# Kernel tuning notes

Hardware: AMD Instinct MI355X
Metric: run time of the kernel (lower is better)

## Reference

```python
import jax, jax.numpy as jnp
import numpy as np

B, D, O = 65536, 512, 64   # batch, input_size, output_size
E, T, K = 8, 2, 2          # num_experts, n_task, top-k
H1, H2 = 64, 32            # expert_hidden_layers (hardcoded in Expert)
LOSS_COEF = 0.01
EPS = 1e-10


def setup_inputs() -> dict:
    key = jax.random.key(0)
    ks = jax.random.split(key, 8)
    f32 = jnp.float32
    def rn(k, shape, scale):
        return jax.random.normal(k, shape, f32) * scale
    return {
        "x": jax.random.normal(ks[0], (B, D), f32),
        # gating params (one per task); init random so top-k routing is nontrivial
        "w_gates": rn(ks[1], (T, D, E), 0.02),
        "b_gates": jnp.zeros((T, E), f32),
        # per-expert MLP params, stacked over the expert axis
        "W1": rn(ks[2], (E, D, H1), 1.0 / np.sqrt(D)),
        "b1": jnp.zeros((E, H1), f32),
        "W2": rn(ks[3], (E, H1, H2), 1.0 / np.sqrt(H1)),
        "b2": jnp.zeros((E, H2), f32),
        "W3": rn(ks[4], (E, H2, O), 1.0 / np.sqrt(H2)),
        "b3": jnp.zeros((E, O), f32),
    }


def _cv_squared(v):
    # torch .var() default is unbiased (ddof=1)
    return jnp.var(v, ddof=1) / (jnp.mean(v) ** 2 + EPS)


def reference(x, w_gates, b_gates, W1, b1, W2, b2, W3, b3):
    # --- noisy_top_k_gating in eval mode (train=False): clean logits, top-k softmax ---
    logits = jnp.einsum("bd,tde->tbe", x, w_gates) + b_gates[:, None, :]  # [T,B,E]
    top_v, top_i = jax.lax.top_k(logits, K)                                # [T,B,K]
    top_g = jax.nn.softmax(top_v, axis=-1)                                 # [T,B,K]
    # scatter top-k gate values back to dense [T,B,E] (zeros elsewhere)
    gates = jnp.sum(jax.nn.one_hot(top_i, E, dtype=top_g.dtype) * top_g[..., None], axis=2)

    # --- experts: each token through each expert MLP (gates zero out non-selected,
    #     mathematically identical to dispatch/combine) ---
    h = jax.nn.relu(jnp.einsum("bd,edh->ebh", x, W1) + b1[:, None, :])     # [E,B,H1]
    h = jax.nn.relu(jnp.einsum("ebh,eho->ebo", h, W2) + b2[:, None, :])    # [E,B,H2]
    expert_out = jax.nn.relu(jnp.einsum("ebh,eho->ebo", h, W3) + b3[:, None, :])  # [E,B,O]

    # weighted combine per task
    y = jnp.einsum("tbe,ebo->tbo", gates, expert_out)                       # [T,B,O]

    # --- load balancing loss ---
    importance = gates.sum(axis=1)                          # [T,E]
    load = (gates > 0).sum(axis=1).astype(jnp.float32)      # [T,E]
    loss = LOSS_COEF * (jax.vmap(_cv_squared)(importance) + jax.vmap(_cv_squared)(load)).sum()
    return y, loss
```

## Files before the change

### kernel.cpp

```cpp
#include <hip/hip_runtime.h>


typedef short bfrag __attribute__((ext_vector_type(8)));
typedef float facc  __attribute__((ext_vector_type(4)));

#define MFMA16(a, b, c) __builtin_amdgcn_mfma_f32_16x16x32_bf16((a), (b), (c), 0, 0, 0)

__device__ __forceinline__ unsigned short bfbits(float f) {
  unsigned int u = __builtin_bit_cast(unsigned int, f);
  u += 0x7FFFu + ((u >> 16) & 1u);
  return (unsigned short)(u >> 16);
}
__device__ __forceinline__ unsigned pack2(float a, float b) {
  return (unsigned)bfbits(a) | ((unsigned)bfbits(b) << 16);
}
__device__ __forceinline__ float bf2f(unsigned short s) {
  unsigned int u = ((unsigned int)s) << 16;
  return __builtin_bit_cast(float, u);
}

#define G_OFF   65536
#define R_OFF   70656
#define A_OFF   72704
#define SM_SIZE 72832

__global__ __launch_bounds__(512, 4) void moe_fused(
    const float* __restrict__ x,
    const float* __restrict__ b_gates,
    const float* __restrict__ wgt,
    const float* __restrict__ b1,
    const float* __restrict__ b2,
    const float* __restrict__ b3,
    const bfrag* __restrict__ w1f,
    const bfrag* __restrict__ w2f,
    const bfrag* __restrict__ w3f,
    float* __restrict__ gacc_out,
    float* __restrict__ y)
{
  __shared__ alignas(16) char smem[SM_SIZE];
  const int tid = threadIdx.x;
  const int wave = tid >> 6, lane = tid & 63;
  const int q = lane & 15, g = lane >> 4;
  const int e = wave;
  const unsigned cb = (unsigned)e * 8192u;

  if (tid < 32) ((float*)(smem + A_OFF))[tid] = 0.f;

  const float* src = x + (size_t)blockIdx.x * 64 * 512 + lane * 512 + wave * 64;
  float4 fr[16];
  #pragma unroll
  for (int j = 0; j < 16; ++j) fr[j] = ((const float4*)src)[j];

  {
    int wu = __builtin_amdgcn_readfirstlane(wave);
    const float* wbase = wgt + wu * 64;
    float* pp = (float*)(smem + wave * 4096 + lane * 64);
    #pragma unroll
    for (int te = 0; te < 16; ++te) {
      const float* wrow = wbase + te * 512;
      float a0 = 0.f, a1 = 0.f, a2 = 0.f, a3 = 0.f;
      #pragma unroll
      for (int j = 0; j < 16; ++j) {
        a0 = fmaf(fr[j].x, wrow[j * 4 + 0], a0);
        a1 = fmaf(fr[j].y, wrow[j * 4 + 1], a1);
        a2 = fmaf(fr[j].z, wrow[j * 4 + 2], a2);
        a3 = fmaf(fr[j].w, wrow[j * 4 + 3], a3);
      }
      pp[(te + lane) & 15] = (a0 + a1) + (a2 + a3);
    }
  }
  __syncthreads();

  #pragma unroll
  for (int i0 = 0; i0 < 2; ++i0) {
    int i = i0 * 512 + tid;
    int tok = i >> 4, te = i & 15;
    const float* pb = (const float*)smem + tok * 16 + ((te + tok) & 15);
    float s = 0.f;
    #pragma unroll
    for (int w2 = 0; w2 < 8; ++w2) s += pb[w2 * 1024];
    ((float*)(smem + G_OFF))[tok * 20 + te] = s + b_gates[te];
  }
  __syncthreads();

  #pragma unroll
  for (int p = 0; p < 8; ++p) {
    uint4 v;
    v.x = pack2(fr[2 * p].x, fr[2 * p].y);
    v.y = pack2(fr[2 * p].z, fr[2 * p].w);
    v.z = pack2(fr[2 * p + 1].x, fr[2 * p + 1].y);
    v.w = pack2(fr[2 * p + 1].z, fr[2 * p + 1].w);
    unsigned byte = ((unsigned)(lane * 1024 + wave * 128 + p * 16)) ^ ((unsigned)(lane & 7) << 4);
    *(uint4*)(smem + byte) = v;
  }

  if (tid < 128) {
    int tok = tid >> 1, task = tid & 1;
    const float* Gr = (const float*)(smem + G_OFF) + tok * 20 + task * 8;
    float l[8];
    #pragma unroll
    for (int ee = 0; ee < 8; ++ee) l[ee] = Gr[ee];
    float v1 = l[0]; int e1 = 0;
    #pragma unroll
    for (int ee = 1; ee < 8; ++ee) { if (l[ee] > v1) { v1 = l[ee]; e1 = ee; } }
    float v2 = -3.4e38f; int e2 = 0;
    #pragma unroll
    for (int ee = 0; ee < 8; ++ee) {
      if (ee != e1 && l[ee] > v2) { v2 = l[ee]; e2 = ee; }
    }
    float g1 = 1.f / (1.f + __expf(v2 - v1));
    float g2 = 1.f - g1;
    float4 rec;
    rec.x = g1; rec.y = g2;
    rec.z = __int_as_float(e1); rec.w = __int_as_float(e2);
    ((float4*)(smem + R_OFF))[tok * 2 + task] = rec;
    float* lacc = (float*)(smem + A_OFF);
    atomicAdd(lacc + task * 8 + e1, g1);
    atomicAdd(lacc + task * 8 + e2, g2);
    atomicAdd(lacc + 16 + task * 8 + e1, 1.f);
    atomicAdd(lacc + 16 + task * 8 + e2, 1.f);
  }
  __syncthreads();

  facc acc[4][4];
  #pragma unroll
  for (int m = 0; m < 4; ++m)
    #pragma unroll
    for (int n = 0; n < 4; ++n) acc[m][n] = (facc)0.f;

  const bfrag* w1e = w1f + e * 4096 + lane;
  #pragma unroll
  for (int ks = 0; ks < 16; ++ks) {
    bfrag A[4];
    #pragma unroll
    for (int m = 0; m < 4; ++m) {
      unsigned ba = ((unsigned)((m * 16 + q) * 1024 + ks * 64 + g * 16)) ^ ((unsigned)(q & 7) << 4);
      A[m] = *(const bfrag*)(smem + ba);
    }
    #pragma unroll
    for (int n = 0; n < 4; ++n) {
      bfrag B = w1e[ks * 256 + n * 64];
      #pragma unroll
      for (int m = 0; m < 4; ++m) acc[m][n] = MFMA16(A[m], B, acc[m][n]);
    }
  }
  __syncthreads();

  {
    float bv[4];
    #pragma unroll
    for (int n = 0; n < 4; ++n) bv[n] = b1[e * 64 + n * 16 + q];
    #pragma unroll
    for (int m = 0; m < 4; ++m) {
      #pragma unroll
      for (int j = 0; j < 4; ++j) {
        float v0 = fmaxf(acc[m][0][j] + bv[0], 0.f);
        float v1 = fmaxf(acc[m][1][j] + bv[1], 0.f);
        float v2 = fmaxf(acc[m][2][j] + bv[2], 0.f);
        float v3 = fmaxf(acc[m][3][j] + bv[3], 0.f);
        int rr = m * 16 + g * 4 + j;
        unsigned byte = cb + (((unsigned)(rr * 128 + q * 8)) ^ ((unsigned)(rr & 7) << 4));
        uint2 p; p.x = pack2(v0, v1); p.y = pack2(v2, v3);
        *(uint2*)(smem + byte) = p;
      }
    }
  }

  {
    facc a2[4][2];
    #pragma unroll
    for (int m = 0; m < 4; ++m) { a2[m][0] = (facc)0.f; a2[m][1] = (facc)0.f; }
    const bfrag* w2e = w2f + e * 256 + lane;
    #pragma unroll
    for (int ks = 0; ks < 2; ++ks) {
      bfrag A[4];
      #pragma unroll
      for (int m = 0; m < 4; ++m) {
        unsigned ba = cb + (((unsigned)((m * 16 + q) * 128 + ks * 64 + g * 16)) ^ ((unsigned)(q & 7) << 4));
        A[m] = *(const bfrag*)(smem + ba);
      }
      #pragma unroll
      for (int n = 0; n < 2; ++n) {
        bfrag B = w2e[ks * 128 + n * 64];
        #pragma unroll
        for (int m = 0; m < 4; ++m) a2[m][n] = MFMA16(A[m], B, a2[m][n]);
      }
    }
    float bv0 = b2[e * 32 + q];
    float bv1 = b2[e * 32 + 16 + q];
    #pragma unroll
    for (int m = 0; m < 4; ++m) {
      #pragma unroll
      for (int j = 0; j < 4; ++j) {
        float v0 = fmaxf(a2[m][0][j] + bv0, 0.f);
        float v1 = fmaxf(a2[m][1][j] + bv1, 0.f);
        int rr = m * 16 + g * 4 + j;
        unsigned byte = cb + (((unsigned)(rr * 64 + q * 4)) ^ ((unsigned)(rr & 7) << 4));
        *(unsigned int*)(smem + byte) = pack2(v0, v1);
      }
    }
  }

  {
    facc a3[4][4];
    #pragma unroll
    for (int m = 0; m < 4; ++m)
      #pragma unroll
      for (int n = 0; n < 4; ++n) a3[m][n] = (facc)0.f;
    const bfrag* w3e = w3f + e * 256 + lane;
    bfrag A[4];
    #pragma unroll
    for (int m = 0; m < 4; ++m) {
      unsigned ba = cb + (((unsigned)((m * 16 + q) * 64 + g * 16)) ^ ((unsigned)(q & 7) << 4));
      A[m] = *(const bfrag*)(smem + ba);
    }
    #pragma unroll
    for (int n = 0; n < 4; ++n) {
      bfrag B = w3e[n * 64];
      #pragma unroll
      for (int m = 0; m < 4; ++m) a3[m][n] = MFMA16(A[m], B, a3[m][n]);
    }
    float bv[4];
    #pragma unroll
    for (int n = 0; n < 4; ++n) bv[n] = b3[e * 64 + n * 16 + q];
    #pragma unroll
    for (int m = 0; m < 4; ++m) {
      #pragma unroll
      for (int j = 0; j < 4; ++j) {
        float v0 = fmaxf(a3[m][0][j] + bv[0], 0.f);
        float v1 = fmaxf(a3[m][1][j] + bv[1], 0.f);
        float v2 = fmaxf(a3[m][2][j] + bv[2], 0.f);
        float v3 = fmaxf(a3[m][3][j] + bv[3], 0.f);
        int rr = m * 16 + g * 4 + j;
        unsigned byte = cb + (((unsigned)(rr * 128 + q * 8)) ^ ((unsigned)(rr & 7) << 4));
        uint2 p; p.x = pack2(v0, v1); p.y = pack2(v2, v3);
        *(uint2*)(smem + byte) = p;
      }
    }
  }
  __syncthreads();

  {
    int tsub = tid >> 4, u = tid & 15;
    const float4* recs = (const float4*)(smem + R_OFF);
    #pragma unroll
    for (int half = 0; half < 2; ++half) {
      int tok = tsub + half * 32;
      size_t trow = (size_t)blockIdx.x * 64 + tok;
      unsigned obyte = ((unsigned)(tok * 128 + u * 8)) ^ ((unsigned)(tok & 7) << 4);
      #pragma unroll
      for (int tt = 0; tt < 2; ++tt) {
        float4 rec = recs[tok * 2 + tt];
        float g1 = rec.x, g2 = rec.y;
        int e1 = __float_as_int(rec.z), e2 = __float_as_int(rec.w);
        uint2 o1 = *(const uint2*)(smem + e1 * 8192 + obyte);
        uint2 o2 = *(const uint2*)(smem + e2 * 8192 + obyte);
        unsigned short s1[4] = { (unsigned short)o1.x, (unsigned short)(o1.x >> 16),
                                 (unsigned short)o1.y, (unsigned short)(o1.y >> 16) };
        unsigned short s2[4] = { (unsigned short)o2.x, (unsigned short)(o2.x >> 16),
                                 (unsigned short)o2.y, (unsigned short)(o2.y >> 16) };
        float* yt = y + (size_t)tt * 4194304 + trow * 64;
        #pragma unroll
        for (int w = 0; w < 4; ++w) {
          yt[w * 16 + u] = g1 * bf2f(s1[w]) + g2 * bf2f(s2[w]);
        }
      }
    }
  }
  if (tid < 32) atomicAdd(gacc_out + tid, ((float*)(smem + A_OFF))[tid]);
}

__global__ __launch_bounds__(256) void moe_prep(
    const float* __restrict__ W1, const float* __restrict__ W2,
    const float* __restrict__ W3, const float* __restrict__ wg,
    bfrag* __restrict__ w1f, bfrag* __restrict__ w2f,
    bfrag* __restrict__ w3f, float* __restrict__ wgt,
    float* __restrict__ gacc)
{
  int tid = blockIdx.x * 256 + threadIdx.x;
  bfrag o;
  if (tid < 32768) {
    int lane = tid & 63, nt = (tid >> 6) & 3, ks = (tid >> 8) & 15, e = tid >> 12;
    int q = lane & 15, g = lane >> 4;
    int hcol = nt * 16 + q;
    #pragma unroll
    for (int j = 0; j < 8; ++j) {
      int k = ks * 32 + g * 8 + j;
      o[j] = (short)bfbits(W1[((e * 512 + k) * 64) + hcol]);
    }
    w1f[tid] = o;
  } else if (tid < 34816) {
    int idx = tid - 32768;
    int lane = idx & 63, nt = (idx >> 6) & 1, ks = (idx >> 7) & 1, e = idx >> 8;
    int q = lane & 15, g = lane >> 4;
    int n = nt * 16 + q;
    #pragma unroll
    for (int j = 0; j < 8; ++j) {
      int s = ks * 32 + g * 8 + j;
      int hh = (s & 3) * 16 + (s >> 2);
      o[j] = (short)bfbits(W2[(e * 64 + hh) * 32 + n]);
    }
    w2f[idx] = o;
  } else if (tid < 36864) {
    int idx = tid - 34816;
    int lane = idx & 63, nt = (idx >> 6) & 3, e = idx >> 8;
    int q = lane & 15, g = lane >> 4;
    int ocol = nt * 16 + q;
    #pragma unroll
    for (int j = 0; j < 8; ++j) {
      int s = g * 8 + j;
      int hh = (s & 1) * 16 + (s >> 1);
      o[j] = (short)bfbits(W3[(e * 32 + hh) * 64 + ocol]);
    }
    w3f[idx] = o;
  } else if (tid < 45056) {
    int idx = tid - 36864;
    int te = idx >> 9, k = idx & 511;
    wgt[idx] = wg[(((te >> 3) * 512) + k) * 8 + (te & 7)];
  } else if (tid < 45088) {
    gacc[tid - 45056] = 0.f;
  }
}

__global__ void moe_loss(const float* __restrict__ acc, float* __restrict__ out) {
  if (threadIdx.x == 0 && blockIdx.x == 0) {
    float loss = 0.f;
    for (int a = 0; a < 4; ++a) {
      const float* v = acc + a * 8;
      float m = 0.f;
      for (int i = 0; i < 8; ++i) m += v[i];
      m *= 0.125f;
      float var = 0.f;
      for (int i = 0; i < 8; ++i) { float d = v[i] - m; var += d * d; }
      var *= (1.f / 7.f);
      loss += var / (m * m + 1e-10f);
    }
    out[8388608] = 0.01f * loss;
  }
}

extern "C" void kernel_launch(void* const* d_in, const int* in_sizes, int n_in,
                              void* d_out, int out_size, void* d_ws, size_t ws_size,
                              hipStream_t stream) {
  const float* x  = (const float*)d_in[0];
  const float* wg = (const float*)d_in[1];
  const float* bg = (const float*)d_in[2];
  const float* W1 = (const float*)d_in[3];
  const float* b1 = (const float*)d_in[4];
  const float* W2 = (const float*)d_in[5];
  const float* b2 = (const float*)d_in[6];
  const float* W3 = (const float*)d_in[7];
  const float* b3 = (const float*)d_in[8];
  float* y = (float*)d_out;

  char* ws = (char*)d_ws;
  float*  gacc = (float*)ws;
  bfrag*  w1f  = (bfrag*)(ws + 128);
  bfrag*  w2f  = (bfrag*)(ws + 524416);
  bfrag*  w3f  = (bfrag*)(ws + 557184);
  float*  wgt  = (float*)(ws + 589952);

  moe_prep<<<177, 256, 0, stream>>>(W1, W2, W3, wg, w1f, w2f, w3f, wgt, gacc);
  moe_fused<<<1024, 512, 0, stream>>>(x, bg, wgt, b1, b2, b3, w1f, w2f, w3f, gacc, y);
  moe_loss<<<1, 64, 0, stream>>>(gacc, y);
}
```

Measured before the change: 96.82 us.

## Halve tokens per block, reduce gating via shuffles, raise occupancy

```diff
diff --git a/kernel.cpp b/kernel.cpp
--- a/kernel.cpp
+++ b/kernel.cpp
@@ -19,12 +19,12 @@
   return __builtin_bit_cast(float, u);
 }
 
-#define G_OFF   65536
-#define R_OFF   70656
-#define A_OFF   72704
-#define SM_SIZE 72832
-
-__global__ __launch_bounds__(512, 4) void moe_fused(
+#define G_OFF   32768
+#define R_OFF   34816
+#define A_OFF   35840
+#define SM_SIZE 35968
+
+__global__ __launch_bounds__(512, 6) void moe_fused(
     const float* __restrict__ x,
     const float* __restrict__ b_gates,
     const float* __restrict__ wgt,
@@ -42,61 +42,61 @@
   const int wave = tid >> 6, lane = tid & 63;
   const int q = lane & 15, g = lane >> 4;
   const int e = wave;
-  const unsigned cb = (unsigned)e * 8192u;
+  const unsigned cb = (unsigned)e * 4096u;
+  const int tok = tid >> 4;
+  const int kg  = tid & 15;
 
   if (tid < 32) ((float*)(smem + A_OFF))[tid] = 0.f;
 
-  const float* src = x + (size_t)blockIdx.x * 64 * 512 + lane * 512 + wave * 64;
-  float4 fr[16];
-  #pragma unroll
-  for (int j = 0; j < 16; ++j) fr[j] = ((const float4*)src)[j];
-
-  {
-    int wu = __builtin_amdgcn_readfirstlane(wave);
-    const float* wbase = wgt + wu * 64;
-    float* pp = (float*)(smem + wave * 4096 + lane * 64);
+  const float* xrow = x + (size_t)blockIdx.x * 32 * 512 + tok * 512 + kg * 4;
+  float4 fr[8];
+  #pragma unroll
+  for (int j = 0; j < 8; ++j) fr[j] = *(const float4*)(xrow + j * 64);
+
+  float p[16];
+  {
+    const float* wbase = wgt + kg * 4;
     #pragma unroll
     for (int te = 0; te < 16; ++te) {
       const float* wrow = wbase + te * 512;
       float a0 = 0.f, a1 = 0.f, a2 = 0.f, a3 = 0.f;
       #pragma unroll
-      for (int j = 0; j < 16; ++j) {
-        a0 = fmaf(fr[j].x, wrow[j * 4 + 0], a0);
-        a1 = fmaf(fr[j].y, wrow[j * 4 + 1], a1);
-        a2 = fmaf(fr[j].z, wrow[j * 4 + 2], a2);
-        a3 = fmaf(fr[j].w, wrow[j * 4 + 3], a3);
-      }
-      pp[(te + lane) & 15] = (a0 + a1) + (a2 + a3);
-    }
+      for (int j = 0; j < 8; ++j) {
+        float4 w4 = *(const float4*)(wrow + j * 64);
+        a0 = fmaf(fr[j].x, w4.x, a0);
+        a1 = fmaf(fr[j].y, w4.y, a1);
+        a2 = fmaf(fr[j].z, w4.z, a2);
+        a3 = fmaf(fr[j].w, w4.w, a3);
+      }
+      p[te] = (a0 + a1) + (a2 + a3);
+    }
+  }
+
+  #pragma unroll
+  for (int m = 8; m >= 1; m >>= 1) {
+    #pragma unroll
+    for (int i = 0; i < m; ++i) {
+      float lo = p[i], hi = p[i + m];
+      float lo_r = __shfl_xor(lo, m, 64);
+      float hi_r = __shfl_xor(hi, m, 64);
+      p[i] = (kg & m) ? (hi + hi_r) : (lo + lo_r);
+    }
+  }
+  ((float*)(smem + G_OFF))[tok * 16 + kg] = p[0] + b_gates[kg];
+
+  #pragma unroll
+  for (int j = 0; j < 8; ++j) {
+    uint2 v;
+    v.x = pack2(fr[j].x, fr[j].y);
+    v.y = pack2(fr[j].z, fr[j].w);
+    unsigned byte = ((unsigned)(tok * 1024 + j * 128 + kg * 8)) ^ ((unsigned)(tok & 7) << 4);
+    *(uint2*)(smem + byte) = v;
   }
   __syncthreads();
 
-  #pragma unroll
-  for (int i0 = 0; i0 < 2; ++i0) {
-    int i = i0 * 512 + tid;
-    int tok = i >> 4, te = i & 15;
-    const float* pb = (const float*)smem + tok * 16 + ((te + tok) & 15);
-    float s = 0.f;
-    #pragma unroll
-    for (int w2 = 0; w2 < 8; ++w2) s += pb[w2 * 1024];
-    ((float*)(smem + G_OFF))[tok * 20 + te] = s + b_gates[te];
-  }
-  __syncthreads();
-
-  #pragma unroll
-  for (int p = 0; p < 8; ++p) {
-    uint4 v;
-    v.x = pack2(fr[2 * p].x, fr[2 * p].y);
-    v.y = pack2(fr[2 * p].z, fr[2 * p].w);
-    v.z = pack2(fr[2 * p + 1].x, fr[2 * p + 1].y);
-    v.w = pack2(fr[2 * p + 1].z, fr[2 * p + 1].w);
-    unsigned byte = ((unsigned)(lane * 1024 + wave * 128 + p * 16)) ^ ((unsigned)(lane & 7) << 4);
-    *(uint4*)(smem + byte) = v;
-  }
-
-  if (tid < 128) {
-    int tok = tid >> 1, task = tid & 1;
-    const float* Gr = (const float*)(smem + G_OFF) + tok * 20 + task * 8;
+  if (tid < 64) {
+    int ttok = tid >> 1, task = tid & 1;
+    const float* Gr = (const float*)(smem + G_OFF) + ttok * 16 + task * 8;
     float l[8];
     #pragma unroll
     for (int ee = 0; ee < 8; ++ee) l[ee] = Gr[ee];
@@ -113,35 +113,35 @@
     float4 rec;
     rec.x = g1; rec.y = g2;
     rec.z = __int_as_float(e1); rec.w = __int_as_float(e2);
-    ((float4*)(smem + R_OFF))[tok * 2 + task] = rec;
+    ((float4*)(smem + R_OFF))[ttok * 2 + task] = rec;
     float* lacc = (float*)(smem + A_OFF);
     atomicAdd(lacc + task * 8 + e1, g1);
     atomicAdd(lacc + task * 8 + e2, g2);
     atomicAdd(lacc + 16 + task * 8 + e1, 1.f);
     atomicAdd(lacc + 16 + task * 8 + e2, 1.f);
   }
-  __syncthreads();
-
-  facc acc[4][4];
-  #pragma unroll
-  for (int m = 0; m < 4; ++m)
+
+  facc acc[2][4];
+  #pragma unroll
+  for (int m = 0; m < 2; ++m)
     #pragma unroll
     for (int n = 0; n < 4; ++n) acc[m][n] = (facc)0.f;
 
   const bfrag* w1e = w1f + e * 4096 + lane;
   #pragma unroll
   for (int ks = 0; ks < 16; ++ks) {
-    bfrag A[4];
-    #pragma unroll
-    for (int m = 0; m < 4; ++m) {
-      unsigned ba = ((unsigned)((m * 16 + q) * 1024 + ks * 64 + g * 16)) ^ ((unsigned)(q & 7) << 4);
-      A[m] = *(const bfrag*)(smem + ba);
+    bfrag A0, A1;
+    {
+      unsigned ba0 = ((unsigned)(q * 1024 + ks * 64 + g * 16)) ^ ((unsigned)(q & 7) << 4);
+      unsigned ba1 = ((unsigned)((16 + q) * 1024 + ks * 64 + g * 16)) ^ ((unsigned)(q & 7) << 4);
+      A0 = *(const bfrag*)(smem + ba0);
+      A1 = *(const bfrag*)(smem + ba1);
     }
     #pragma unroll
     for (int n = 0; n < 4; ++n) {
       bfrag B = w1e[ks * 256 + n * 64];
-      #pragma unroll
-      for (int m = 0; m < 4; ++m) acc[m][n] = MFMA16(A[m], B, acc[m][n]);
+      acc[0][n] = MFMA16(A0, B, acc[0][n]);
+      acc[1][n] = MFMA16(A1, B, acc[1][n]);
     }
   }
   __syncthreads();
@@ -151,7 +151,7 @@
     #pragma unroll
     for (int n = 0; n < 4; ++n) bv[n] = b1[e * 64 + n * 16 + q];
     #pragma unroll
-    for (int m = 0; m < 4; ++m) {
+    for (int m = 0; m < 2; ++m) {
       #pragma unroll
       for (int j = 0; j < 4; ++j) {
         float v0 = fmaxf(acc[m][0][j] + bv[0], 0.f);
@@ -160,36 +160,34 @@
         float v3 = fmaxf(acc[m][3][j] + bv[3], 0.f);
         int rr = m * 16 + g * 4 + j;
         unsigned byte = cb + (((unsigned)(rr * 128 + q * 8)) ^ ((unsigned)(rr & 7) << 4));
-        uint2 p; p.x = pack2(v0, v1); p.y = pack2(v2, v3);
-        *(uint2*)(smem + byte) = p;
-      }
-    }
-  }
-
-  {
-    facc a2[4][2];
-    #pragma unroll
-    for (int m = 0; m < 4; ++m) { a2[m][0] = (facc)0.f; a2[m][1] = (facc)0.f; }
+        uint2 pk; pk.x = pack2(v0, v1); pk.y = pack2(v2, v3);
+        *(uint2*)(smem + byte) = pk;
+      }
+    }
+  }
+
+  {
+    facc a2[2][2];
+    #pragma unroll
+    for (int m = 0; m < 2; ++m) { a2[m][0] = (facc)0.f; a2[m][1] = (facc)0.f; }
     const bfrag* w2e = w2f + e * 256 + lane;
     #pragma unroll
     for (int ks = 0; ks < 2; ++ks) {
-      bfrag A[4];
-      #pragma unroll
-      for (int m = 0; m < 4; ++m) {
-        unsigned ba = cb + (((unsigned)((m * 16 + q) * 128 + ks * 64 + g * 16)) ^ ((unsigned)(q & 7) << 4));
-        A[m] = *(const bfrag*)(smem + ba);
-      }
+      unsigned ba0 = cb + (((unsigned)(q * 128 + ks * 64 + g * 16)) ^ ((unsigned)(q & 7) << 4));
+      unsigned ba1 = cb + (((unsigned)((16 + q) * 128 + ks * 64 + g * 16)) ^ ((unsigned)(q & 7) << 4));
+      bfrag A0 = *(const bfrag*)(smem + ba0);
+      bfrag A1 = *(const bfrag*)(smem + ba1);
       #pragma unroll
       for (int n = 0; n < 2; ++n) {
         bfrag B = w2e[ks * 128 + n * 64];
-        #pragma unroll
-        for (int m = 0; m < 4; ++m) a2[m][n] = MFMA16(A[m], B, a2[m][n]);
+        a2[0][n] = MFMA16(A0, B, a2[0][n]);
+        a2[1][n] = MFMA16(A1, B, a2[1][n]);
       }
     }
     float bv0 = b2[e * 32 + q];
     float bv1 = b2[e * 32 + 16 + q];
     #pragma unroll
-    for (int m = 0; m < 4; ++m) {
+    for (int m = 0; m < 2; ++m) {
       #pragma unroll
       for (int j = 0; j < 4; ++j) {
         float v0 = fmaxf(a2[m][0][j] + bv0, 0.f);
@@ -202,29 +200,27 @@
   }
 
   {
-    facc a3[4][4];
-    #pragma unroll
-    for (int m = 0; m < 4; ++m)
+    facc a3[2][4];
+    #pragma unroll
+    for (int m = 0; m < 2; ++m)
       #pragma unroll
       for (int n = 0; n < 4; ++n) a3[m][n] = (facc)0.f;
     const bfrag* w3e = w3f + e * 256 + lane;
-    bfrag A[4];
-    #pragma unroll
-    for (int m = 0; m < 4; ++m) {
-      unsigned ba = cb + (((unsigned)((m * 16 + q) * 64 + g * 16)) ^ ((unsigned)(q & 7) << 4));
-      A[m] = *(const bfrag*)(smem + ba);
-    }
+    unsigned ba0 = cb + (((unsigned)(q * 64 + g * 16)) ^ ((unsigned)(q & 7) << 4));
+    unsigned ba1 = cb + (((unsigned)((16 + q) * 64 + g * 16)) ^ ((unsigned)(q & 7) << 4));
+    bfrag A0 = *(const bfrag*)(smem + ba0);
+    bfrag A1 = *(const bfrag*)(smem + ba1);
     #pragma unroll
     for (int n = 0; n < 4; ++n) {
       bfrag B = w3e[n * 64];
-      #pragma unroll
-      for (int m = 0; m < 4; ++m) a3[m][n] = MFMA16(A[m], B, a3[m][n]);
+      a3[0][n] = MFMA16(A0, B, a3[0][n]);
+      a3[1][n] = MFMA16(A1, B, a3[1][n]);
     }
     float bv[4];
     #pragma unroll
     for (int n = 0; n < 4; ++n) bv[n] = b3[e * 64 + n * 16 + q];
     #pragma unroll
-    for (int m = 0; m < 4; ++m) {
+    for (int m = 0; m < 2; ++m) {
       #pragma unroll
       for (int j = 0; j < 4; ++j) {
         float v0 = fmaxf(a3[m][0][j] + bv[0], 0.f);
@@ -233,37 +229,33 @@
         float v3 = fmaxf(a3[m][3][j] + bv[3], 0.f);
         int rr = m * 16 + g * 4 + j;
         unsigned byte = cb + (((unsigned)(rr * 128 + q * 8)) ^ ((unsigned)(rr & 7) << 4));
-        uint2 p; p.x = pack2(v0, v1); p.y = pack2(v2, v3);
-        *(uint2*)(smem + byte) = p;
+        uint2 pk; pk.x = pack2(v0, v1); pk.y = pack2(v2, v3);
+        *(uint2*)(smem + byte) = pk;
       }
     }
   }
   __syncthreads();
 
   {
-    int tsub = tid >> 4, u = tid & 15;
+    int u = kg;
+    size_t trow = (size_t)blockIdx.x * 32 + tok;
+    unsigned obyte = ((unsigned)(tok * 128 + u * 8)) ^ ((unsigned)(tok & 7) << 4);
     const float4* recs = (const float4*)(smem + R_OFF);
     #pragma unroll
-    for (int half = 0; half < 2; ++half) {
-      int tok = tsub + half * 32;
-      size_t trow = (size_t)blockIdx.x * 64 + tok;
-      unsigned obyte = ((unsigned)(tok * 128 + u * 8)) ^ ((unsigned)(tok & 7) << 4);
-      #pragma unroll
-      for (int tt = 0; tt < 2; ++tt) {
-        float4 rec = recs[tok * 2 + tt];
-        float g1 = rec.x, g2 = rec.y;
-        int e1 = __float_as_int(rec.z), e2 = __float_as_int(rec.w);
-        uint2 o1 = *(const uint2*)(smem + e1 * 8192 + obyte);
-        uint2 o2 = *(const uint2*)(smem + e2 * 8192 + obyte);
-        unsigned short s1[4] = { (unsigned short)o1.x, (unsigned short)(o1.x >> 16),
-                                 (unsigned short)o1.y, (unsigned short)(o1.y >> 16) };
-        unsigned short s2[4] = { (unsigned short)o2.x, (unsigned short)(o2.x >> 16),
-                                 (unsigned short)o2.y, (unsigned short)(o2.y >> 16) };
-        float* yt = y + (size_t)tt * 4194304 + trow * 64;
-        #pragma unroll
-        for (int w = 0; w < 4; ++w) {
-          yt[w * 16 + u] = g1 * bf2f(s1[w]) + g2 * bf2f(s2[w]);
-        }
+    for (int tt = 0; tt < 2; ++tt) {
+      float4 rec = recs[tok * 2 + tt];
+      float g1 = rec.x, g2 = rec.y;
+      int e1 = __float_as_int(rec.z), e2 = __float_as_int(rec.w);
+      uint2 o1 = *(const uint2*)(smem + e1 * 4096 + obyte);
+      uint2 o2 = *(const uint2*)(smem + e2 * 4096 + obyte);
+      unsigned short s1[4] = { (unsigned short)o1.x, (unsigned short)(o1.x >> 16),
+                               (unsigned short)o1.y, (unsigned short)(o1.y >> 16) };
+      unsigned short s2[4] = { (unsigned short)o2.x, (unsigned short)(o2.x >> 16),
+                               (unsigned short)o2.y, (unsigned short)(o2.y >> 16) };
+      float* yt = y + (size_t)tt * 4194304 + trow * 64;
+      #pragma unroll
+      for (int w = 0; w < 4; ++w) {
+        yt[w * 16 + u] = g1 * bf2f(s1[w]) + g2 * bf2f(s2[w]);
       }
     }
   }
@@ -361,6 +353,6 @@
   float*  wgt  = (float*)(ws + 589952);
 
   moe_prep<<<177, 256, 0, stream>>>(W1, W2, W3, wg, w1f, w2f, w3f, wgt, gacc);
-  moe_fused<<<1024, 512, 0, stream>>>(x, bg, wgt, b1, b2, b3, w1f, w2f, w3f, gacc, y);
+  moe_fused<<<2048, 512, 0, stream>>>(x, bg, wgt, b1, b2, b3, w1f, w2f, w3f, gacc, y);
   moe_loss<<<1, 64, 0, stream>>>(gacc, y);
 }
```

New measurement: 341.7 us. 3.53x slower.

## Prefetch expert weights into registers and fold loss into fused kernel

Applied to the files above, without the earlier changes.

```diff
diff --git a/kernel.cpp b/kernel.cpp
--- a/kernel.cpp
+++ b/kernel.cpp
@@ -129,21 +129,33 @@
     for (int n = 0; n < 4; ++n) acc[m][n] = (facc)0.f;
 
   const bfrag* w1e = w1f + e * 4096 + lane;
+  bfrag Bc[4], Bn[4];
+  #pragma unroll
+  for (int n = 0; n < 4; ++n) Bc[n] = w1e[n * 64];
   #pragma unroll
   for (int ks = 0; ks < 16; ++ks) {
-    bfrag A[4];
+    if (ks < 15) {
+      #pragma unroll
+      for (int n = 0; n < 4; ++n) Bn[n] = w1e[(ks + 1) * 256 + n * 64];
+    }
     #pragma unroll
     for (int m = 0; m < 4; ++m) {
       unsigned ba = ((unsigned)((m * 16 + q) * 1024 + ks * 64 + g * 16)) ^ ((unsigned)(q & 7) << 4);
-      A[m] = *(const bfrag*)(smem + ba);
-    }
-    #pragma unroll
-    for (int n = 0; n < 4; ++n) {
-      bfrag B = w1e[ks * 256 + n * 64];
-      #pragma unroll
-      for (int m = 0; m < 4; ++m) acc[m][n] = MFMA16(A[m], B, acc[m][n]);
-    }
-  }
+      bfrag A = *(const bfrag*)(smem + ba);
+      #pragma unroll
+      for (int n = 0; n < 4; ++n) acc[m][n] = MFMA16(A, Bc[n], acc[m][n]);
+    }
+    if (ks < 15) {
+      #pragma unroll
+      for (int n = 0; n < 4; ++n) Bc[n] = Bn[n];
+    }
+  }
+
+  bfrag W2r[4];
+  #pragma unroll
+  for (int i = 0; i < 4; ++i) W2r[i] = w2f[e * 256 + i * 64 + lane];
+  float b2v0 = b2[e * 32 + q];
+  float b2v1 = b2[e * 32 + 16 + q];
   __syncthreads();
 
   {
@@ -170,67 +182,55 @@
     facc a2[4][2];
     #pragma unroll
     for (int m = 0; m < 4; ++m) { a2[m][0] = (facc)0.f; a2[m][1] = (facc)0.f; }
-    const bfrag* w2e = w2f + e * 256 + lane;
     #pragma unroll
     for (int ks = 0; ks < 2; ++ks) {
-      bfrag A[4];
       #pragma unroll
       for (int m = 0; m < 4; ++m) {
         unsigned ba = cb + (((unsigned)((m * 16 + q) * 128 + ks * 64 + g * 16)) ^ ((unsigned)(q & 7) << 4));
-        A[m] = *(const bfrag*)(smem + ba);
-      }
-      #pragma unroll
-      for (int n = 0; n < 2; ++n) {
-        bfrag B = w2e[ks * 128 + n * 64];
+        bfrag A = *(const bfrag*)(smem + ba);
         #pragma unroll
-        for (int m = 0; m < 4; ++m) a2[m][n] = MFMA16(A[m], B, a2[m][n]);
-      }
-    }
-    float bv0 = b2[e * 32 + q];
-    float bv1 = b2[e * 32 + 16 + q];
+        for (int n = 0; n < 2; ++n) a2[m][n] = MFMA16(A, W2r[ks * 2 + n], a2[m][n]);
+      }
+    }
+    bfrag W3r[4];
+    #pragma unroll
+    for (int n = 0; n < 4; ++n) W3r[n] = w3f[e * 256 + n * 64 + lane];
+    float b3v[4];
+    #pragma unroll
+    for (int n = 0; n < 4; ++n) b3v[n] = b3[e * 64 + n * 16 + q];
+
     #pragma unroll
     for (int m = 0; m < 4; ++m) {
       #pragma unroll
       for (int j = 0; j < 4; ++j) {
-        float v0 = fmaxf(a2[m][0][j] + bv0, 0.f);
-        float v1 = fmaxf(a2[m][1][j] + bv1, 0.f);
+        float v0 = fmaxf(a2[m][0][j] + b2v0, 0.f);
+        float v1 = fmaxf(a2[m][1][j] + b2v1, 0.f);
         int rr = m * 16 + g * 4 + j;
         unsigned byte = cb + (((unsigned)(rr * 64 + q * 4)) ^ ((unsigned)(rr & 7) << 4));
         *(unsigned int*)(smem + byte) = pack2(v0, v1);
       }
     }
-  }
-
-  {
+
     facc a3[4][4];
     #pragma unroll
     for (int m = 0; m < 4; ++m)
       #pragma unroll
       for (int n = 0; n < 4; ++n) a3[m][n] = (facc)0.f;
-    const bfrag* w3e = w3f + e * 256 + lane;
-    bfrag A[4];
     #pragma unroll
     for (int m = 0; m < 4; ++m) {
       unsigned ba = cb + (((unsigned)((m * 16 + q) * 64 + g * 16)) ^ ((unsigned)(q & 7) << 4));
-      A[m] = *(const bfrag*)(smem + ba);
-    }
-    #pragma unroll
-    for (int n = 0; n < 4; ++n) {
-      bfrag B = w3e[n * 64];
-      #pragma unroll
-      for (int m = 0; m < 4; ++m) a3[m][n] = MFMA16(A[m], B, a3[m][n]);
-    }
-    float bv[4];
-    #pragma unroll
-    for (int n = 0; n < 4; ++n) bv[n] = b3[e * 64 + n * 16 + q];
+      bfrag A = *(const bfrag*)(smem + ba);
+      #pragma unroll
+      for (int n = 0; n < 4; ++n) a3[m][n] = MFMA16(A, W3r[n], a3[m][n]);
+    }
     #pragma unroll
     for (int m = 0; m < 4; ++m) {
       #pragma unroll
       for (int j = 0; j < 4; ++j) {
-        float v0 = fmaxf(a3[m][0][j] + bv[0], 0.f);
-        float v1 = fmaxf(a3[m][1][j] + bv[1], 0.f);
-        float v2 = fmaxf(a3[m][2][j] + bv[2], 0.f);
-        float v3 = fmaxf(a3[m][3][j] + bv[3], 0.f);
+        float v0 = fmaxf(a3[m][0][j] + b3v[0], 0.f);
+        float v1 = fmaxf(a3[m][1][j] + b3v[1], 0.f);
+        float v2 = fmaxf(a3[m][2][j] + b3v[2], 0.f);
+        float v3 = fmaxf(a3[m][3][j] + b3v[3], 0.f);
         int rr = m * 16 + g * 4 + j;
         unsigned byte = cb + (((unsigned)(rr * 128 + q * 8)) ^ ((unsigned)(rr & 7) << 4));
         uint2 p; p.x = pack2(v0, v1); p.y = pack2(v2, v3);
@@ -268,6 +268,31 @@
     }
   }
   if (tid < 32) atomicAdd(gacc_out + tid, ((float*)(smem + A_OFF))[tid]);
+  __syncthreads();
+
+  if (tid == 0) {
+    unsigned* cnt = (unsigned*)(gacc_out + 32);
+    unsigned old = atomicAdd(cnt, 1u);
+    if (old == gridDim.x - 1) {
+      float loss = 0.f;
+      #pragma unroll
+      for (int a = 0; a < 4; ++a) {
+        float v[8]; float mm = 0.f;
+        #pragma unroll
+        for (int i = 0; i < 8; ++i) {
+          v[i] = __hip_atomic_load(gacc_out + a * 8 + i, __ATOMIC_RELAXED,
+                                   __HIP_MEMORY_SCOPE_AGENT);
+          mm += v[i];
+        }
+        mm *= 0.125f;
+        float var = 0.f;
+        #pragma unroll
+        for (int i = 0; i < 8; ++i) { float d = v[i] - mm; var += d * d; }
+        loss += (var * (1.f / 7.f)) / (mm * mm + 1e-10f);
+      }
+      y[8388608] = 0.01f * loss;
+    }
+  }
 }
 
 __global__ __launch_bounds__(256) void moe_prep(
@@ -317,25 +342,8 @@
     int idx = tid - 36864;
     int te = idx >> 9, k = idx & 511;
     wgt[idx] = wg[(((te >> 3) * 512) + k) * 8 + (te & 7)];
-  } else if (tid < 45088) {
+  } else if (tid < 45089) {
     gacc[tid - 45056] = 0.f;
-  }
-}
-
-__global__ void moe_loss(const float* __restrict__ acc, float* __restrict__ out) {
-  if (threadIdx.x == 0 && blockIdx.x == 0) {
-    float loss = 0.f;
-    for (int a = 0; a < 4; ++a) {
-      const float* v = acc + a * 8;
-      float m = 0.f;
-      for (int i = 0; i < 8; ++i) m += v[i];
-      m *= 0.125f;
-      float var = 0.f;
-      for (int i = 0; i < 8; ++i) { float d = v[i] - m; var += d * d; }
-      var *= (1.f / 7.f);
-      loss += var / (m * m + 1e-10f);
-    }
-    out[8388608] = 0.01f * loss;
   }
 }
 
@@ -355,12 +363,11 @@
 
   char* ws = (char*)d_ws;
   float*  gacc = (float*)ws;
-  bfrag*  w1f  = (bfrag*)(ws + 128);
-  bfrag*  w2f  = (bfrag*)(ws + 524416);
-  bfrag*  w3f  = (bfrag*)(ws + 557184);
-  float*  wgt  = (float*)(ws + 589952);
+  bfrag*  w1f  = (bfrag*)(ws + 256);
+  bfrag*  w2f  = (bfrag*)(ws + 524544);
+  bfrag*  w3f  = (bfrag*)(ws + 557312);
+  float*  wgt  = (float*)(ws + 590080);
 
   moe_prep<<<177, 256, 0, stream>>>(W1, W2, W3, wg, w1f, w2f, w3f, wgt, gacc);
   moe_fused<<<1024, 512, 0, stream>>>(x, bg, wgt, b1, b2, b3, w1f, w2f, w3f, gacc, y);
-  moe_loss<<<1, 64, 0, stream>>>(gacc, y);
-}
+}
```

Measured after the change: 87.75 us (median of 4 runs). 1.1x faster.
